# Performance work log

Measured on AMD Instinct MI355X. Metric: run time of the kernel, lower is better.

Reference implementation:

```python
import jax, jax.numpy as jnp
import numpy as np

HIDDEN = 256
EMB = 256
SEQ_LEN = 256  # = input_size, the decode loop bound


def setup_inputs() -> dict:
    key = jax.random.key(0)
    ks = jax.random.split(key, 8)
    B, T_enc, OUT = 512, 64, 256
    s = 1.0 / np.sqrt(HIDDEN)
    return {
        "input": jax.random.normal(ks[0], (B, SEQ_LEN), dtype=jnp.float32),
        "encoder_output": jax.random.normal(ks[1], (B, T_enc, HIDDEN), dtype=jnp.float32),
        "W_ih": jax.random.normal(ks[2], (4 * HIDDEN, EMB), dtype=jnp.float32) * s,
        "b_ih": jax.random.normal(ks[3], (4 * HIDDEN,), dtype=jnp.float32) * s,
        "W_hh": jax.random.normal(ks[4], (4 * HIDDEN, HIDDEN), dtype=jnp.float32) * s,
        "b_hh": jax.random.normal(ks[5], (4 * HIDDEN,), dtype=jnp.float32) * s,
        "W2": jax.random.normal(ks[6], (OUT, HIDDEN), dtype=jnp.float32) * s,
        "b2": jax.random.normal(ks[7], (OUT,), dtype=jnp.float32) * s,
    }


def reference(input, encoder_output, W_ih, b_ih, W_hh, b_hh, W2, b2):
    B = input.shape[0]
    # init_state: transpose(1,0) then last -> last encoder timestep, fixed cell input every step
    cell_state = encoder_output[:, -1, :]                      # [B, H]
    # decoder_input is zeros [B, E] every step -> input-gate contribution is constant
    x_part = jnp.zeros((B, EMB), input.dtype) @ W_ih.T + b_ih  # [B, 4H]

    def step(h, _):
        # NOTE: torch LSTMCell returns (h', c'); source assigns out=h', hidden=c',
        # so next step's h-input is the previous CELL state; c-input stays cell_state.
        gates = x_part + h @ W_hh.T + b_hh                     # [B, 4H]
        i, f, g, o = jnp.split(gates, 4, axis=-1)
        i, f, o = jax.nn.sigmoid(i), jax.nn.sigmoid(f), jax.nn.sigmoid(o)
        g = jnp.tanh(g)
        c_new = f * cell_state + i * g
        h_new = o * jnp.tanh(c_new)
        prob = jax.nn.softmax(h_new @ W2.T + b2, axis=-1)      # [B, OUT]
        return c_new, prob

    h0 = jnp.zeros((B, HIDDEN), input.dtype)
    _, probs = jax.lax.scan(step, h0, None, length=SEQ_LEN)    # [S, B, OUT]
    return jnp.transpose(probs, (1, 0, 2))                     # [B, S, OUT]
```

## Files before the change

kernel.cpp:

```cpp
#include <hip/hip_runtime.h>
#include <math.h>
#include <stdint.h>

typedef float f32x4 __attribute__((ext_vector_type(4)));

__device__ __forceinline__ float sigm(float x) { return 1.0f/(1.0f+expf(-x)); }

__device__ __forceinline__ float red8(float v) {
    int t;
    t = __builtin_amdgcn_update_dpp(0, __float_as_int(v), 0xB1, 0xf, 0xf, false);
    v += __int_as_float(t);
    t = __builtin_amdgcn_update_dpp(0, __float_as_int(v), 0x4E, 0xf, 0xf, false);
    v += __int_as_float(t);
    t = __builtin_amdgcn_update_dpp(0, __float_as_int(v), 0x141, 0xf, 0xf, false);
    v += __int_as_float(t);
    return v;
}

__global__ __launch_bounds__(1024) void rec_kernel(
    const float* __restrict__ enc,
    const float* __restrict__ b_ih,
    const float* __restrict__ W_hh,
    const float* __restrict__ b_hh,
    float* __restrict__ hstage)
{
    const int tid  = threadIdx.x;
    const int wv   = tid >> 6;
    const int lane = tid & 63;
    const int kseg = lane & 7;
    const int r8   = lane >> 3;
    const int half = wv >> 3;
    const int wg   = wv & 7;
    const int rloc = 8*wg + r8;
    const int b0   = blockIdx.x * 2;

    __shared__ float part[2][2][1024];
    __shared__ float h_lds[2][256];

    const int pj = tid & 255;
    const int ph = (tid >> 8) & 1;
    float c0 = 0.f, pb0 = 0.f, pb1 = 0.f, pb2 = 0.f, pb3 = 0.f;
    float* __restrict__ outp = nullptr;
    if (tid < 512) {
        c0  = enc[(size_t)(b0 + ph)*16384 + 16128 + pj];
        pb0 = b_ih[      pj] + b_hh[      pj];
        pb1 = b_ih[256 + pj] + b_hh[256 + pj];
        pb2 = b_ih[512 + pj] + b_hh[512 + pj];
        pb3 = b_ih[768 + pj] + b_hh[768 + pj];
        outp = hstage + (size_t)(b0 + ph)*65536 + pj;
    }

    const float* __restrict__ wbase =
        W_hh + (size_t)rloc*256 + half*128 + kseg*4;

    #define LOADP(q0, q1, q2, q3, pm) do {                           \
        const float* wp_ = wbase + (size_t)(pm)*16384;               \
        q0 = *(const f32x4*)(wp_     );                              \
        q1 = *(const f32x4*)(wp_ + 32);                              \
        q2 = *(const f32x4*)(wp_ + 64);                              \
        q3 = *(const f32x4*)(wp_ + 96);                              \
    } while (0)

    #define COMPUTE(q0, q1, q2, q3, p) do {                          \
        f32x4 s0 = q0*h00; f32x4 s1 = q0*h10;                        \
        s0 += q1*h01;      s1 += q1*h11;                             \
        s0 += q2*h02;      s1 += q2*h12;                             \
        s0 += q3*h03;      s1 += q3*h13;                             \
        float a0 = (s0.x + s0.y) + (s0.z + s0.w);                    \
        float a1 = (s1.x + s1.y) + (s1.z + s1.w);                    \
        a0 = red8(a0); a1 = red8(a1);                                \
        if (kseg == 0) {                                             \
            const int grow_ = (p)*64 + rloc;                         \
            part[half][0][grow_] = a0;                               \
            part[half][1][grow_] = a1;                               \
        }                                                            \
    } while (0)

    f32x4 h00 = (f32x4)(0.f), h01 = (f32x4)(0.f),
          h02 = (f32x4)(0.f), h03 = (f32x4)(0.f);
    f32x4 h10 = (f32x4)(0.f), h11 = (f32x4)(0.f),
          h12 = (f32x4)(0.f), h13 = (f32x4)(0.f);

    f32x4 wA0, wA1, wA2, wA3, wB0, wB1, wB2, wB3;

    LOADP(wA0, wA1, wA2, wA3, 0);
    LOADP(wB0, wB1, wB2, wB3, 1);

    for (int t = 0; t < 256; ++t) {
        #pragma unroll 1
        for (int pq = 0; pq < 8; ++pq) {
            const int p = pq*2;
            COMPUTE(wA0, wA1, wA2, wA3, p    );
            LOADP(wA0, wA1, wA2, wA3, (p + 2) & 15);
            COMPUTE(wB0, wB1, wB2, wB3, p + 1);
            LOADP(wB0, wB1, wB2, wB3, (p + 3) & 15);
        }
        asm volatile("s_waitcnt lgkmcnt(0)" ::: "memory");
        __builtin_amdgcn_s_barrier();

        if (tid < 512) {
            const float g0 = part[0][ph][      pj] + part[1][ph][      pj] + pb0;
            const float g1 = part[0][ph][256 + pj] + part[1][ph][256 + pj] + pb1;
            const float g2 = part[0][ph][512 + pj] + part[1][ph][512 + pj] + pb2;
            const float g3 = part[0][ph][768 + pj] + part[1][ph][768 + pj] + pb3;
            const float cn = sigm(g1)*c0 + sigm(g0)*tanhf(g2);
            const float hn = sigm(g3)*tanhf(cn);
            h_lds[ph][pj] = cn;
            __builtin_nontemporal_store(hn, outp + t*256);
        }
        asm volatile("s_waitcnt lgkmcnt(0)" ::: "memory");
        __builtin_amdgcn_s_barrier();

        h00 = *(const f32x4*)&h_lds[0][half*128 + kseg*4     ];
        h01 = *(const f32x4*)&h_lds[0][half*128 + kseg*4 + 32];
        h02 = *(const f32x4*)&h_lds[0][half*128 + kseg*4 + 64];
        h03 = *(const f32x4*)&h_lds[0][half*128 + kseg*4 + 96];
        h10 = *(const f32x4*)&h_lds[1][half*128 + kseg*4     ];
        h11 = *(const f32x4*)&h_lds[1][half*128 + kseg*4 + 32];
        h12 = *(const f32x4*)&h_lds[1][half*128 + kseg*4 + 64];
        h13 = *(const f32x4*)&h_lds[1][half*128 + kseg*4 + 96];
    }
    #undef LOADP
    #undef COMPUTE
}

__global__ __launch_bounds__(1024) void out_kernel(
    const float* __restrict__ W2,
    const float* __restrict__ b2,
    float* __restrict__ io)
{
    const int tid = threadIdx.x;
    const int rg  = tid & 15;
    const int cg  = tid >> 4;
    const int m0  = blockIdx.x * 64;

    __shared__ float tile[64][260];

    #pragma unroll
    for (int i = 0; i < 4; ++i) {
        const int idx = tid + i*1024;
        const int r   = idx >> 6;
        const int c4  = idx & 63;
        const f32x4 v = __builtin_nontemporal_load(
            (const f32x4*)(io + (size_t)(m0 + r)*256 + c4*4));
        *(f32x4*)&tile[r][c4*4] = v;
    }
    __syncthreads();

    float b2v[4];
    #pragma unroll
    for (int ci = 0; ci < 4; ++ci) b2v[ci] = b2[cg*4 + ci];

    float acc[4][4] = {};

    #pragma unroll 4
    for (int k4 = 0; k4 < 64; ++k4) {
        const f32x4 h0 = *(const f32x4*)&tile[rg     ][k4*4];
        const f32x4 h1 = *(const f32x4*)&tile[rg + 16][k4*4];
        const f32x4 h2 = *(const f32x4*)&tile[rg + 32][k4*4];
        const f32x4 h3 = *(const f32x4*)&tile[rg + 48][k4*4];
        #pragma unroll
        for (int ci = 0; ci < 4; ++ci) {
            const f32x4 wv = *(const f32x4*)(W2 + (size_t)(cg*4 + ci)*256 + k4*4);
            acc[0][ci] += wv.x*h0.x + wv.y*h0.y + wv.z*h0.z + wv.w*h0.w;
            acc[1][ci] += wv.x*h1.x + wv.y*h1.y + wv.z*h1.z + wv.w*h1.w;
            acc[2][ci] += wv.x*h2.x + wv.y*h2.y + wv.z*h2.z + wv.w*h2.w;
            acc[3][ci] += wv.x*h3.x + wv.y*h3.y + wv.z*h3.z + wv.w*h3.w;
        }
    }
    __syncthreads();

    #pragma unroll
    for (int ri = 0; ri < 4; ++ri) {
        f32x4 v;
        v.x = acc[ri][0] + b2v[0];
        v.y = acc[ri][1] + b2v[1];
        v.z = acc[ri][2] + b2v[2];
        v.w = acc[ri][3] + b2v[3];
        *(f32x4*)&tile[rg + 16*ri][cg*4] = v;
    }
    __syncthreads();

    const int wv_ = tid >> 6;
    const int l   = tid & 63;
    #pragma unroll
    for (int rr2 = 0; rr2 < 4; ++rr2) {
        const int r = wv_*4 + rr2;
        const float v0 = tile[r][l      ];
        const float v1 = tile[r][l +  64];
        const float v2 = tile[r][l + 128];
        const float v3 = tile[r][l + 192];
        float m = fmaxf(fmaxf(v0, v1), fmaxf(v2, v3));
        #pragma unroll
        for (int off = 32; off > 0; off >>= 1)
            m = fmaxf(m, __shfl_xor(m, off));
        const float e0 = expf(v0 - m), e1 = expf(v1 - m);
        const float e2 = expf(v2 - m), e3 = expf(v3 - m);
        float s = e0 + e1 + e2 + e3;
        #pragma unroll
        for (int off = 32; off > 0; off >>= 1)
            s += __shfl_xor(s, off);
        const float inv = 1.0f / s;
        float* op = io + (size_t)(m0 + r)*256;
        __builtin_nontemporal_store(e0*inv, op + l      );
        __builtin_nontemporal_store(e1*inv, op + l +  64);
        __builtin_nontemporal_store(e2*inv, op + l + 128);
        __builtin_nontemporal_store(e3*inv, op + l + 192);
    }
}

extern "C" void kernel_launch(void* const* d_in, const int* in_sizes, int n_in,
                              void* d_out, int out_size, void* d_ws, size_t ws_size,
                              hipStream_t stream) {
    const float* enc  = (const float*)d_in[1];
    const float* b_ih = (const float*)d_in[3];
    const float* W_hh = (const float*)d_in[4];
    const float* b_hh = (const float*)d_in[5];
    const float* W2   = (const float*)d_in[6];
    const float* b2   = (const float*)d_in[7];
    float* outp = (float*)d_out;

    hipLaunchKernelGGL(rec_kernel, dim3(256), dim3(1024), 0, stream,
                       enc, b_ih, W_hh, b_hh, outp);
    hipLaunchKernelGGL(out_kernel, dim3(2048), dim3(1024), 0, stream,
                       W2, b2, outp);
}
```

Before: 2.557 ms.

## Keep part of W_hh resident in registers and LDS across timesteps

The recurrent kernel used to stream all 16 row-panels of W_hh from global memory/L2 on every timestep. Now four panels stay in registers and two more in padded LDS for the whole loop, so only ten panels are still streamed with the double-buffered loads. The aim is less per-step global load traffic and latency on the serial recurrence. In exchange it uses about 133KB of LDS and 16 extra vector registers per thread at 1024 threads, which raises the risk of spills or of exceeding the LDS limit.

Result: slower. 3.794 ms (+48.4%).

```diff
diff --git a/kernel.cpp b/kernel.cpp
--- a/kernel.cpp
+++ b/kernel.cpp
@@ -34,6 +34,7 @@
     const int rloc = 8*wg + r8;
     const int b0   = blockIdx.x * 2;
 
+    __shared__ __align__(16) float Wlds[2][64*260];
     __shared__ float part[2][2][1024];
     __shared__ float h_lds[2][256];
 
@@ -76,24 +77,57 @@
         }                                                            \
     } while (0)
 
+    #define COMPUTE_L(li, p) do {                                    \
+        const float* wl_ = &Wlds[li][rloc*260 + half*128 + kseg*4];  \
+        const f32x4 t0 = *(const f32x4*)(wl_     );                  \
+        const f32x4 t1 = *(const f32x4*)(wl_ + 32);                  \
+        const f32x4 t2 = *(const f32x4*)(wl_ + 64);                  \
+        const f32x4 t3 = *(const f32x4*)(wl_ + 96);                  \
+        COMPUTE(t0, t1, t2, t3, p);                                  \
+    } while (0)
+
     f32x4 h00 = (f32x4)(0.f), h01 = (f32x4)(0.f),
           h02 = (f32x4)(0.f), h03 = (f32x4)(0.f);
     f32x4 h10 = (f32x4)(0.f), h11 = (f32x4)(0.f),
           h12 = (f32x4)(0.f), h13 = (f32x4)(0.f);
 
+    f32x4 rA0, rA1, rA2, rA3, rB0, rB1, rB2, rB3;
+    f32x4 rC0, rC1, rC2, rC3, rD0, rD1, rD2, rD3;
+    LOADP(rA0, rA1, rA2, rA3, 12);
+    LOADP(rB0, rB1, rB2, rB3, 13);
+    LOADP(rC0, rC1, rC2, rC3, 14);
+    LOADP(rD0, rD1, rD2, rD3, 15);
+
+    for (int s = tid; s < 2*64*64; s += 1024) {
+        const int li  = s >> 12;
+        const int rem = s & 4095;
+        const int row = rem >> 6;
+        const int c4  = rem & 63;
+        *(f32x4*)&Wlds[li][row*260 + c4*4] =
+            *(const f32x4*)&W_hh[(size_t)(10 + li)*16384 + row*256 + c4*4];
+    }
+
     f32x4 wA0, wA1, wA2, wA3, wB0, wB1, wB2, wB3;
-
     LOADP(wA0, wA1, wA2, wA3, 0);
     LOADP(wB0, wB1, wB2, wB3, 1);
 
+    __syncthreads();
+
     for (int t = 0; t < 256; ++t) {
+        COMPUTE(rA0, rA1, rA2, rA3, 12);
+        COMPUTE(rB0, rB1, rB2, rB3, 13);
+        COMPUTE(rC0, rC1, rC2, rC3, 14);
+        COMPUTE(rD0, rD1, rD2, rD3, 15);
+        COMPUTE_L(0, 10);
+        COMPUTE_L(1, 11);
         #pragma unroll 1
-        for (int pq = 0; pq < 8; ++pq) {
-            const int p = pq*2;
-            COMPUTE(wA0, wA1, wA2, wA3, p    );
-            LOADP(wA0, wA1, wA2, wA3, (p + 2) & 15);
-            COMPUTE(wB0, wB1, wB2, wB3, p + 1);
-            LOADP(wB0, wB1, wB2, wB3, (p + 3) & 15);
+        for (int sp = 0; sp < 10; sp += 2) {
+            int pm2 = sp + 2; if (pm2 >= 10) pm2 -= 10;
+            int pm3 = sp + 3; if (pm3 >= 10) pm3 -= 10;
+            COMPUTE(wA0, wA1, wA2, wA3, sp    );
+            LOADP(wA0, wA1, wA2, wA3, pm2);
+            COMPUTE(wB0, wB1, wB2, wB3, sp + 1);
+            LOADP(wB0, wB1, wB2, wB3, pm3);
         }
         asm volatile("s_waitcnt lgkmcnt(0)" ::: "memory");
         __builtin_amdgcn_s_barrier();
@@ -122,6 +156,7 @@
     }
     #undef LOADP
     #undef COMPUTE
+    #undef COMPUTE_L
 }
 
 __global__ __launch_bounds__(1024) void out_kernel(
```
